# Kernel tuning notes

Hardware: AMD Instinct MI355X
Metric: run time of the kernel (lower is better)

## Reference

```python
import jax, jax.numpy as jnp
import numpy as np
from jax import lax

B, N, M = 16, 4096, 1024
RADII = [0.1, 0.2]
KS = [32, 64]
MLP_SPECS = [[64, 64, 128], [64, 96, 128]]
C_IN = 64 + 3  # use_xyz
EPS = 1e-5


def setup_inputs() -> dict:
    key = jax.random.key(0)
    ks = jax.random.split(key, 32)
    inp = {
        "pc": jax.random.uniform(ks[0], (B, 3, N), jnp.float32),
        "features": jax.random.normal(ks[1], (B, 64, N), jnp.float32),
    }
    ki = 2
    for i, spec in enumerate(MLP_SPECS):
        cin = C_IN
        for j, cout in enumerate(spec):
            inp[f"W{i}{j}"] = jax.random.normal(ks[ki], (cout, cin), jnp.float32) * (1.0 / np.sqrt(cin)); ki += 1
            inp[f"b{i}{j}"] = jnp.zeros((cout,), jnp.float32)
            inp[f"g{i}{j}"] = jnp.ones((cout,), jnp.float32)
            inp[f"be{i}{j}"] = jnp.zeros((cout,), jnp.float32)
            cin = cout
    return inp


def farthest_point_sampling(pc_t, m):
    # pc_t: [B, N, 3] -> [B, m] int32 indices. Sequential FPS via scan.
    b, n, _ = pc_t.shape
    init = (jnp.full((b, n), 1e10, pc_t.dtype), jnp.zeros((b,), jnp.int32))
    def step(carry, _):
        dmin, far = carry
        centroid = jnp.take_along_axis(pc_t, far[:, None, None], axis=1)  # [B,1,3]
        dist = jnp.sum((pc_t - centroid) ** 2, axis=-1)                    # [B,N]
        dmin = jnp.minimum(dmin, dist)
        nxt = jnp.argmax(dmin, axis=-1).astype(jnp.int32)
        return (dmin, nxt), far
    _, idxs = lax.scan(step, init, None, length=m)
    return idxs.T  # [B, m]


def ball_query(pc_t, centers_t, r, k):
    # pc_t: [B,N,3], centers_t: [B,M,3] -> [B,M,k] int32.
    # Original CUDA semantics: first k points (in index order) within radius;
    # pad with the first found index if fewer than k.
    n = pc_t.shape[1]
    d2 = jnp.sum((centers_t[:, :, None, :] - pc_t[:, None, :, :]) ** 2, axis=-1)  # [B,M,N]
    cand = jnp.where(d2 < r * r, jnp.arange(n, dtype=jnp.int32), jnp.int32(n))
    neg, _ = lax.top_k(-cand, k)   # k smallest candidate indices
    idx = -neg
    first = idx[:, :, :1]
    return jnp.where(idx == n, first, idx)


def group_points(feat, idx):
    # feat: [B,C,N], idx: [B,M,K] -> [B,C,M,K]
    return jax.vmap(lambda f, i: f[:, i])(feat, idx)


def _mlp_bn_relu(x, params):
    # x: [B,C,M,K]; 1x1 conv == channel matmul, BN over (B,M,K) (training stats), ReLU
    for (W, b, g, be) in params:
        x = jnp.einsum('oc,bcmk->bomk', W, x) + b[None, :, None, None]
        mu = jnp.mean(x, axis=(0, 2, 3), keepdims=True)
        var = jnp.var(x, axis=(0, 2, 3), keepdims=True)
        x = (x - mu) * lax.rsqrt(var + EPS) * g[None, :, None, None] + be[None, :, None, None]
        x = jax.nn.relu(x)
    return x


def _forward(pc, features, params):
    pc_t = pc.transpose(0, 2, 1)                       # [B,N,3]
    samp = farthest_point_sampling(pc_t, M)            # [B,M]
    new_pc = jnp.take_along_axis(pc, jnp.broadcast_to(samp[:, None, :], (B, 3, M)), axis=2)  # [B,3,M]
    new_pc_t = new_pc.transpose(0, 2, 1)               # [B,M,3]
    outs = []
    for i in range(len(RADII)):
        gidx = ball_query(pc_t, new_pc_t, RADII[i], KS[i])          # [B,M,K]
        xyz = group_points(pc, gidx) - new_pc[:, :, :, None]        # [B,3,M,K]
        grp = group_points(features, gidx)                          # [B,64,M,K]
        x = jnp.concatenate([xyz, grp], axis=1)                     # [B,67,M,K]
        x = _mlp_bn_relu(x, params[i])
        outs.append(jnp.max(x, axis=-1))                            # [B,Cout,M]
    return new_pc, jnp.concatenate(outs, axis=1)


def reference(pc, features,
              W00, b00, g00, be00, W01, b01, g01, be01, W02, b02, g02, be02,
              W10, b10, g10, be10, W11, b11, g11, be11, W12, b12, g12, be12):
    params = [
        [(W00, b00, g00, be00), (W01, b01, g01, be01), (W02, b02, g02, be02)],
        [(W10, b10, g10, be10), (W11, b11, g11, be11), (W12, b12, g12, be12)],
    ]
    return _forward(pc, features, params)
```

## Files before the change

### kernel.cpp

```cpp
#include <hip/hip_runtime.h>
#include <cstdio>
#include <cstdint>


constexpr int BATCH = 16, NPTS = 4096, MCTR = 1024;
constexpr int BM = BATCH * MCTR;
constexpr int NSLOT = 32;

typedef short bf16x8 __attribute__((ext_vector_type(8)));
typedef float f32x4  __attribute__((ext_vector_type(4)));
typedef float f32x2  __attribute__((ext_vector_type(2)));

__device__ __forceinline__ ushort f2bf(float f) {
  uint32_t u = __float_as_uint(f);
  u += 0x7fffu + ((u >> 16) & 1u);
  return (ushort)(u >> 16);
}
__device__ __forceinline__ uint32_t packbf(float a, float b) {
  return (uint32_t)f2bf(a) | ((uint32_t)f2bf(b) << 16);
}
__device__ __forceinline__ unsigned long long umax64(unsigned long long a,
                                                     unsigned long long b) {
  return (a > b) ? a : b;
}

template <int CTRL>
__device__ __forceinline__ unsigned long long dpp_max(unsigned long long k) {
  int lo = (int)(uint32_t)k, hi = (int)(uint32_t)(k >> 32);
  uint32_t plo = (uint32_t)__builtin_amdgcn_update_dpp(0, lo, CTRL, 0xf, 0xf, false);
  uint32_t phi = (uint32_t)__builtin_amdgcn_update_dpp(0, hi, CTRL, 0xf, 0xf, false);
  unsigned long long pk = ((unsigned long long)phi << 32) | plo;
  return (pk > k) ? pk : k;
}

__device__ __forceinline__ void fps_body(int b, int t, const float* __restrict__ pc,
                                         float* __restrict__ newpc_out,
                                         char* __restrict__ smem) {
  float* lX = (float*)smem;
  float* lY = lX + NPTS;
  float* lZ = lY + NPTS;
  int*   sampL = (int*)(smem + 3 * NPTS * 4);
  unsigned long long* wkey =
      (unsigned long long*)(smem + 3 * NPTS * 4 + MCTR * 4);
  const int lane = t & 63;
  const int w = t >> 6;
  const float* px = pc + (size_t)b * 3 * NPTS;
  f32x2 X2[8], Y2[8], Z2[8], D2[8];
#pragma unroll
  for (int j = 0; j < 16; j++) {
    int p = t + 256 * j;
    float x = px[p], y = px[NPTS + p], z = px[2 * NPTS + p];
    X2[j >> 1][j & 1] = x; Y2[j >> 1][j & 1] = y; Z2[j >> 1][j & 1] = z;
    D2[j >> 1][j & 1] = 1e10f;
    lX[p] = x; lY[p] = y; lZ[p] = z;
  }
  if (t == 0) sampL[0] = 0;
  __syncthreads();
  int far = 0;
  for (int it = 1; it < MCTR; it++) {
    float cx = lX[far], cy = lY[far], cz = lZ[far];
    float bv = -1.0f; int bi = 0;
    {
#pragma clang fp contract(off)
      f32x2 cx2 = {cx, cx}, cy2 = {cy, cy}, cz2 = {cz, cz};
#pragma unroll
      for (int j2 = 0; j2 < 8; j2++) {
        f32x2 dx = X2[j2] - cx2, dy = Y2[j2] - cy2, dz = Z2[j2] - cz2;
        f32x2 d = dx * dx + dy * dy + dz * dz;
        f32x2 dm;
        dm[0] = fminf(D2[j2][0], d[0]);
        dm[1] = fminf(D2[j2][1], d[1]);
        D2[j2] = dm;
        bool g0 = dm[0] > bv;
        bv = g0 ? dm[0] : bv; bi = g0 ? t + 256 * (2 * j2) : bi;
        bool g1 = dm[1] > bv;
        bv = g1 ? dm[1] : bv; bi = g1 ? t + 256 * (2 * j2 + 1) : bi;
      }
    }
    unsigned long long key =
        ((unsigned long long)__float_as_uint(bv) << 32) | (unsigned)(~bi);
    key = dpp_max<0xB1>(key);
    key = dpp_max<0x4E>(key);
    key = dpp_max<0x124>(key);
    key = dpp_max<0x128>(key);
    key = dpp_max<0x142>(key);
    key = dpp_max<0x143>(key);
    if (lane == 63) wkey[(it & 1) * 4 + w] = key;
    __syncthreads();
    const ulonglong2* kp = (const ulonglong2*)(wkey + (it & 1) * 4);
    ulonglong2 k0 = kp[0], k1 = kp[1];
    unsigned long long kk = umax64(umax64(k0.x, k0.y), umax64(k1.x, k1.y));
    far = (int)(~(unsigned)kk);
    if (t == 0) sampL[it] = far;
  }
  __syncthreads();
  float* npc = newpc_out + (size_t)b * 3 * MCTR;
  for (int m = t; m < MCTR; m += 256) {
    int f = sampL[m];
    npc[m] = lX[f]; npc[MCTR + m] = lY[f]; npc[2 * MCTR + m] = lZ[f];
  }
}

__device__ __forceinline__ void u_body(const float* __restrict__ feat,
                                       const float* __restrict__ W,
                                       const float* __restrict__ bias,
                                       ushort* __restrict__ Ub, int ub,
                                       char* __restrict__ smem) {
  float* wl = (float*)smem;
  int t = threadIdx.x;
#pragma unroll
  for (int i = 0; i < 16; i++) {
    int r = t + 256 * i;
    wl[r] = W[(r & 63) * 67 + 3 + (r >> 6)];
  }
  __syncthreads();
  int gid = ub * 256 + t;
  int b = gid >> 12, n = gid & 4095;
  float acc[64];
#pragma unroll
  for (int o = 0; o < 64; o++) acc[o] = bias[o];
  const float* fb = feat + (size_t)b * 64 * NPTS + n;
  for (int c = 0; c < 64; c++) {
    float x = fb[(size_t)c * NPTS];
    const f32x4* w4 = (const f32x4*)(wl + c * 64);
#pragma unroll
    for (int q = 0; q < 16; q++) {
      f32x4 wv = w4[q];
      acc[4 * q + 0] = fmaf(wv[0], x, acc[4 * q + 0]);
      acc[4 * q + 1] = fmaf(wv[1], x, acc[4 * q + 1]);
      acc[4 * q + 2] = fmaf(wv[2], x, acc[4 * q + 2]);
      acc[4 * q + 3] = fmaf(wv[3], x, acc[4 * q + 3]);
    }
  }
  uint4* o4 = (uint4*)(Ub + (size_t)gid * 64);
#pragma unroll
  for (int qq = 0; qq < 8; qq++)
    o4[qq] = make_uint4(packbf(acc[8*qq+0], acc[8*qq+1]), packbf(acc[8*qq+2], acc[8*qq+3]),
                        packbf(acc[8*qq+4], acc[8*qq+5]), packbf(acc[8*qq+6], acc[8*qq+7]));
}

__global__ __launch_bounds__(256) void fused_stageA(
    const float* __restrict__ pc, const float* __restrict__ feat,
    const float* __restrict__ W00, const float* __restrict__ b00,
    const float* __restrict__ W01, const float* __restrict__ W02,
    const float* __restrict__ W10, const float* __restrict__ b10,
    const float* __restrict__ W11, const float* __restrict__ W12,
    float* __restrict__ newpc_out, ushort* __restrict__ Ub0,
    ushort* __restrict__ Ub1, float* __restrict__ wt, ushort* __restrict__ wf) {
  __shared__ __align__(16) char smem[3 * NPTS * 4 + MCTR * 4 + 64];
  int bx = blockIdx.x, t = threadIdx.x;
  if (bx < 16) { fps_body(bx, t, pc, newpc_out, smem); return; }
  if (bx < 528) {
    int ub = bx - 16;
    if (ub < 256) u_body(feat, W00, b00, Ub0, ub, smem);
    else          u_body(feat, W10, b10, Ub1, ub - 256, smem);
    return;
  }
  int e = (bx - 528) * 256 + t;
  if (e < 4096) { wt[e] = W00[(e & 63) * 67 + 3 + (e >> 6)]; return; }
  if (e < 4288) { int r = e - 4096; wt[e] = W00[(r & 63) * 67 + (r >> 6)]; return; }
  if (e < 8384) { int r = e - 4288; wt[e] = W10[(r & 63) * 67 + 3 + (r >> 6)]; return; }
  if (e < 8576) { int r = e - 8384; wt[e] = W10[(r & 63) * 67 + (r >> 6)]; return; }
  int e2 = e - 8576;
  if (e2 >= 30720) return;
  const float* W; int CIN, MT, off;
  if (e2 < 4096)       { W = W01; CIN = 64; MT = 4; off = 0; }
  else if (e2 < 12288) { W = W02; CIN = 64; MT = 8; off = 4096; }
  else if (e2 < 18432) { W = W11; CIN = 64; MT = 6; off = 12288; }
  else                 { W = W12; CIN = 96; MT = 8; off = 18432; }
  int r = e2 - off;
  int j = r & 7, lane = (r >> 3) & 63, fm = r >> 9;
  int kc = fm / MT, mt = fm % MT;
  int out_ch = mt * 16 + (lane & 15);
  int in_ch  = kc * 32 + (lane >> 4) * 8 + j;
  wf[e2] = f2bf(W[out_ch * CIN + in_ch]);
}

template <int K>
__device__ __forceinline__ void ballq_body(int bx, const float* __restrict__ pc,
                                           const float* __restrict__ newpc,
                                           int* __restrict__ gidx, float r2) {
  int lane = threadIdx.x & 63;
  int wave = threadIdx.x >> 6;
  int center = bx * 4 + wave;
  int b = center >> 10, m = center & 1023;
  const float* nb = newpc + (size_t)b * 3 * MCTR + m;
  float cx = nb[0], cy = nb[MCTR], cz = nb[2 * MCTR];
  const float* px = pc + (size_t)b * 3 * NPTS;
  int cnt = 0;
  int firstn = 0x7fffffff;
  for (int chunk = 0; chunk < NPTS / 64 && cnt < K; chunk++) {
    int n = chunk * 64 + lane;
    float dx = __fsub_rn(cx, px[n]);
    float dy = __fsub_rn(cy, px[NPTS + n]);
    float dz = __fsub_rn(cz, px[2 * NPTS + n]);
    float d2 = __fadd_rn(__fadd_rn(__fmul_rn(dx, dx), __fmul_rn(dy, dy)), __fmul_rn(dz, dz));
    bool in = d2 < r2;
    unsigned long long ball = __ballot(in);
    int pos = cnt + (int)__popcll(ball & ((1ull << lane) - 1ull));
    if (in && pos < K) gidx[(size_t)center * K + pos] = n;
    if (in && pos == 0) firstn = n;
    cnt += (int)__popcll(ball);
  }
#pragma unroll
  for (int off = 32; off; off >>= 1) firstn = min(firstn, __shfl_xor(firstn, off));
  if (lane < K && lane >= cnt) gidx[(size_t)center * K + lane] = firstn;
}

__global__ __launch_bounds__(256) void ballq_fused(const float* __restrict__ pc,
                                                   const float* __restrict__ newpc,
                                                   int* __restrict__ gidx0,
                                                   int* __restrict__ gidx1,
                                                   float r2a, float r2b) {
  int bx = blockIdx.x;
  if (bx < BM / 4) ballq_body<32>(bx, pc, newpc, gidx0, r2a);
  else             ballq_body<64>(bx - BM / 4, pc, newpc, gidx1, r2b);
}

__device__ __forceinline__ void layer1_compute(const ushort* __restrict__ Ub,
                                               const float* __restrict__ pc,
                                               const float* __restrict__ newpc,
                                               const float* __restrict__ Wt1,
                                               int b, int m, int idx, float* v1) {
  float dx = pc[((size_t)b * 3 + 0) * NPTS + idx] - newpc[((size_t)b * 3 + 0) * MCTR + m];
  float dy = pc[((size_t)b * 3 + 1) * NPTS + idx] - newpc[((size_t)b * 3 + 1) * MCTR + m];
  float dz = pc[((size_t)b * 3 + 2) * NPTS + idx] - newpc[((size_t)b * 3 + 2) * MCTR + m];
  const uint4* u4 = (const uint4*)(Ub + (size_t)((b << 12) + idx) * 64);
#pragma unroll
  for (int qq = 0; qq < 8; qq++) {
    uint4 u = u4[qq];
    v1[8*qq+0] = __uint_as_float(u.x << 16);
    v1[8*qq+1] = __uint_as_float(u.x & 0xffff0000u);
    v1[8*qq+2] = __uint_as_float(u.y << 16);
    v1[8*qq+3] = __uint_as_float(u.y & 0xffff0000u);
    v1[8*qq+4] = __uint_as_float(u.z << 16);
    v1[8*qq+5] = __uint_as_float(u.z & 0xffff0000u);
    v1[8*qq+6] = __uint_as_float(u.w << 16);
    v1[8*qq+7] = __uint_as_float(u.w & 0xffff0000u);
  }
#pragma unroll
  for (int o = 0; o < 64; o++) v1[o] = fmaf(Wt1[o], dx, v1[o]);
#pragma unroll
  for (int o = 0; o < 64; o++) v1[o] = fmaf(Wt1[64 + o], dy, v1[o]);
#pragma unroll
  for (int o = 0; o < 64; o++) v1[o] = fmaf(Wt1[128 + o], dz, v1[o]);
}

__device__ __forceinline__ void wave_reduce32(const float* vals, float* tile, int t,
                                              float* swrow, int co) {
  float* myrow = tile + t * 32;
  int rsw = t & 31;
#pragma unroll
  for (int o = 0; o < 32; o++) myrow[o ^ rsw] = vals[o];
  __syncthreads();
  int lane = t & 63;
  int ch = lane & 31, sub = lane >> 5;
  const float* base = tile + (t & ~63) * 32;
  float s = 0.f, s2 = 0.f;
#pragma unroll
  for (int r = 0; r < 32; r++) {
    int row = sub * 32 + r;
    float v = base[row * 32 + (ch ^ (row & 31))];
    s += v; s2 = fmaf(v, v, s2);
  }
  float st = s + __shfl_xor(s, 32);
  float st2 = s2 + __shfl_xor(s2, 32);
  if (sub == 0) {
    swrow[co + ch] += st;
    swrow[128 + co + ch] += st2;
  }
  __syncthreads();
}

template <int K>
__device__ __forceinline__ void l1_body(
    int bx, const ushort* __restrict__ Ub, const float* __restrict__ pc,
    const float* __restrict__ newpc, const int* __restrict__ gidx,
    const float* __restrict__ Wt1, float* __restrict__ stats,
    float* tile, float* sAcc ) {
  const int t = threadIdx.x;
  const int w = t >> 6;
  const int p = bx * 128 + t;
  const int bm = p / K;
  const int b = bm >> 10, m = bm & 1023;
  const int idx = gidx[p];
  for (int i = t; i < 512; i += 128) sAcc[i] = 0.f;

  float v1[64];
  layer1_compute(Ub, pc, newpc, Wt1, b, m, idx, v1);

  wave_reduce32(v1,      tile, t, sAcc + w * 256, 0);
  wave_reduce32(v1 + 32, tile, t, sAcc + w * 256, 32);

  __syncthreads();
  float* dst = stats + (size_t)(bx & (NSLOT - 1)) * 128;
  for (int i = t; i < 64; i += 128) {
    atomicAdd(&dst[i],      sAcc[i]       + sAcc[256 + i]);
    atomicAdd(&dst[64 + i], sAcc[128 + i] + sAcc[256 + 128 + i]);
  }
}

__global__ __launch_bounds__(128, 2) void l1_fused(
    const ushort* __restrict__ Ub0, const ushort* __restrict__ Ub1,
    const float* __restrict__ pc, const float* __restrict__ newpc,
    const int* __restrict__ gidx0, const int* __restrict__ gidx1,
    const float* __restrict__ Wt1a, const float* __restrict__ Wt1b,
    float* __restrict__ st0, float* __restrict__ st1) {
  __shared__ float tile[128 * 32];
  __shared__ float sAccW[2][256];
  constexpr int NB0 = (BM * 32) / 128;
  int bx = blockIdx.x;
  if (bx < NB0) l1_body<32>(bx, Ub0, pc, newpc, gidx0, Wt1a, st0, tile, &sAccW[0][0]);
  else          l1_body<64>(bx - NB0, Ub1, pc, newpc, gidx1, Wt1b, st1, tile, &sAccW[0][0]);
}

template <int K, int C2, int NL>
__global__ __launch_bounds__(256, 2) void mfma_pass(
    const ushort* __restrict__ Ub, const float* __restrict__ pc,
    const float* __restrict__ newpc, const int* __restrict__ gidx,
    const float* __restrict__ Wt1,
    const ushort* __restrict__ W2f, const ushort* __restrict__ W3f,
    const float* __restrict__ b2, const float* __restrict__ b3,
    const float* __restrict__ cA1, const float* __restrict__ cC1,
    const float* __restrict__ cA2, const float* __restrict__ cC2,
    float* __restrict__ stats, float* __restrict__ maxbuf, float* __restrict__ minbuf) {
  constexpr int MT2 = C2 / 16, KC3 = C2 / 32;
  constexpr int CLs = (NL == 2) ? C2 : 128;
  constexpr int SSTR = CLs + 4;
  __shared__ __align__(16) ushort x1f[4][2][4][64][8];
  __shared__ __align__(16) ushort x2f[(NL == 3) ? 4 : 1][KC3][4][16][8];
  __shared__ __align__(16) ushort x3s[4][16][SSTR];
  __shared__ float sAccW[4][256];

  const int t = threadIdx.x, w = t >> 6, lane = t & 63;
  const int q = lane >> 4, n = lane & 15;
  const int p = blockIdx.x * 256 + t;
  const int bm = p / K;
  const int b = bm >> 10, m = bm & 1023;
  const int idx = gidx[p];

  {
    float v1[64];
    layer1_compute(Ub, pc, newpc, Wt1, b, m, idx, v1);
    int nw = t & 63;
#pragma unroll
    for (int g = 0; g < 8; g++) {
      uint32_t d0, d1, d2, d3;
      int c = g * 8;
      d0 = packbf(fmaxf(0.f, fmaf(cA1[c+0], v1[c+0], cC1[c+0])),
                  fmaxf(0.f, fmaf(cA1[c+1], v1[c+1], cC1[c+1])));
      d1 = packbf(fmaxf(0.f, fmaf(cA1[c+2], v1[c+2], cC1[c+2])),
                  fmaxf(0.f, fmaf(cA1[c+3], v1[c+3], cC1[c+3])));
      d2 = packbf(fmaxf(0.f, fmaf(cA1[c+4], v1[c+4], cC1[c+4])),
                  fmaxf(0.f, fmaf(cA1[c+5], v1[c+5], cC1[c+5])));
      d3 = packbf(fmaxf(0.f, fmaf(cA1[c+6], v1[c+6], cC1[c+6])),
                  fmaxf(0.f, fmaf(cA1[c+7], v1[c+7], cC1[c+7])));
      *(uint4*)&x1f[w][g >> 2][g & 3][nw][0] = make_uint4(d0, d1, d2, d3);
    }
  }
  asm volatile("s_waitcnt lgkmcnt(0)" ::: "memory");

  bf16x8 A2[2 * MT2];
#pragma unroll
  for (int i = 0; i < 2 * MT2; i++) A2[i] = *(const bf16x8*)(W2f + (i * 64 + lane) * 8);
  bf16x8 A3[(NL == 3) ? KC3 * 8 : 1];
  if (NL == 3) {
#pragma unroll
    for (int i = 0; i < KC3 * 8; i++) A3[i] = *(const bf16x8*)(W3f + (i * 64 + lane) * 8);
  }

  float sS0 = 0.f, sS1 = 0.f, sS20 = 0.f, sS21 = 0.f;
  float mx0 = -3.4e38f, mx1 = -3.4e38f, mn0 = 3.4e38f, mn1 = 3.4e38f;

#pragma unroll
  for (int tl = 0; tl < 4; tl++) {
    bf16x8 bf2[2];
#pragma unroll
    for (int kc = 0; kc < 2; kc++)
      bf2[kc] = *(const bf16x8*)&x1f[w][kc][q][tl * 16 + n][0];
    f32x4 acc2[MT2];
#pragma unroll
    for (int mt = 0; mt < MT2; mt++) acc2[mt] = *(const f32x4*)(b2 + mt * 16 + q * 4);
#pragma unroll
    for (int kc = 0; kc < 2; kc++)
#pragma unroll
      for (int mt = 0; mt < MT2; mt++)
        acc2[mt] = __builtin_amdgcn_mfma_f32_16x16x32_bf16(A2[kc * MT2 + mt], bf2[kc],
                                                           acc2[mt], 0, 0, 0);
    if (NL == 2) {
#pragma unroll
      for (int mt = 0; mt < MT2; mt++) {
        int ch0 = mt * 16 + q * 4;
        *(uint2*)&x3s[w][n][ch0] = make_uint2(packbf(acc2[mt][0], acc2[mt][1]),
                                              packbf(acc2[mt][2], acc2[mt][3]));
      }
    } else {
#pragma unroll
      for (int mt = 0; mt < MT2; mt++) {
        int ch0 = mt * 16 + q * 4;
        f32x4 ca = *(const f32x4*)(cA2 + ch0);
        f32x4 cc = *(const f32x4*)(cC2 + ch0);
        float r0 = fmaxf(0.f, fmaf(ca[0], acc2[mt][0], cc[0]));
        float r1 = fmaxf(0.f, fmaf(ca[1], acc2[mt][1], cc[1]));
        float r2 = fmaxf(0.f, fmaf(ca[2], acc2[mt][2], cc[2]));
        float r3 = fmaxf(0.f, fmaf(ca[3], acc2[mt][3], cc[3]));
        int kc2 = ch0 >> 5, q2 = (ch0 >> 3) & 3, j0 = ch0 & 7;
        *(uint2*)&x2f[w][kc2][q2][n][j0] = make_uint2(packbf(r0, r1), packbf(r2, r3));
      }
      asm volatile("s_waitcnt lgkmcnt(0)" ::: "memory");
      f32x4 acc3[8];
#pragma unroll
      for (int mt = 0; mt < 8; mt++) acc3[mt] = *(const f32x4*)(b3 + mt * 16 + q * 4);
#pragma unroll
      for (int kc = 0; kc < KC3; kc++) {
        bf16x8 bf3 = *(const bf16x8*)&x2f[w][kc][q][n][0];
#pragma unroll
        for (int mt = 0; mt < 8; mt++)
          acc3[mt] = __builtin_amdgcn_mfma_f32_16x16x32_bf16(A3[kc * 8 + mt], bf3,
                                                             acc3[mt], 0, 0, 0);
      }
#pragma unroll
      for (int mt = 0; mt < 8; mt++) {
        int ch0 = mt * 16 + q * 4;
        *(uint2*)&x3s[w][n][ch0] = make_uint2(packbf(acc3[mt][0], acc3[mt][1]),
                                              packbf(acc3[mt][2], acc3[mt][3]));
      }
    }
    asm volatile("s_waitcnt lgkmcnt(0)" ::: "memory");
    if (2 * lane < CLs) {
#pragma unroll
      for (int pos = 0; pos < 16; pos++) {
        uint32_t u = *(const uint32_t*)&x3s[w][pos][2 * lane];
        float v0 = __uint_as_float(u << 16);
        float v1v = __uint_as_float(u & 0xffff0000u);
        sS0 += v0;  sS20 = fmaf(v0, v0, sS20);
        sS1 += v1v; sS21 = fmaf(v1v, v1v, sS21);
        if (NL == 3) {
          mx0 = fmaxf(mx0, v0);  mn0 = fminf(mn0, v0);
          mx1 = fmaxf(mx1, v1v); mn1 = fminf(mn1, v1v);
        }
      }
    }
    if (NL == 3) {
      bool fl = (K == 64) ? (tl == 3) : ((tl & 1) == 1);
      if (fl) {
        int center = (K == 64) ? (blockIdx.x * 4 + w)
                               : (blockIdx.x * 8 + w * 2 + (tl >> 1));
        *(float2*)&maxbuf[(size_t)center * 128 + 2 * lane] = make_float2(mx0, mx1);
        *(float2*)&minbuf[(size_t)center * 128 + 2 * lane] = make_float2(mn0, mn1);
        mx0 = mx1 = -3.4e38f; mn0 = mn1 = 3.4e38f;
      }
    }
    asm volatile("s_waitcnt lgkmcnt(0)" ::: "memory");
  }

  {
    int ch = 2 * lane;
    if (ch < CLs) {
      sAccW[w][ch] = sS0;        sAccW[w][ch + 1] = sS1;
      sAccW[w][CLs + ch] = sS20; sAccW[w][CLs + ch + 1] = sS21;
    }
  }
  __syncthreads();
  float* dst = stats + (size_t)(blockIdx.x & (NSLOT - 1)) * (2 * CLs);
  for (int i = t; i < 2 * CLs; i += 256)
    atomicAdd(&dst[i], sAccW[0][i] + sAccW[1][i] + sAccW[2][i] + sAccW[3][i]);
}

__global__ void finalize2_kernel(const float* __restrict__ st0, const float* __restrict__ g0,
                                 const float* __restrict__ be0, float invP0,
                                 float* __restrict__ cAo0, float* __restrict__ cCo0, int C0,
                                 const float* __restrict__ st1, const float* __restrict__ g1,
                                 const float* __restrict__ be1, float invP1,
                                 float* __restrict__ cAo1, float* __restrict__ cCo1, int C1) {
  const float* st = blockIdx.x ? st1 : st0;
  const float* g  = blockIdx.x ? g1  : g0;
  const float* be = blockIdx.x ? be1 : be0;
  float invP = blockIdx.x ? invP1 : invP0;
  float* cA = blockIdx.x ? cAo1 : cAo0;
  float* cC = blockIdx.x ? cCo1 : cCo0;
  int C = blockIdx.x ? C1 : C0;
  int t = threadIdx.x;
  if (t < C) {
    float s = 0.f, s2 = 0.f;
    for (int sl = 0; sl < NSLOT; sl++) {
      s  += st[sl * 2 * C + t];
      s2 += st[sl * 2 * C + C + t];
    }
    float mu = s * invP;
    float var = fmaf(s2, invP, -(mu * mu));
    float a = g[t] / sqrtf(var + 1e-5f);
    cA[t] = a;
    cC[t] = fmaf(-a, mu, be[t]);
  }
}

__global__ __launch_bounds__(256) void outwrite_kernel(const float* __restrict__ maxbuf,
                                                       const float* __restrict__ minbuf,
                                                       const float* __restrict__ cA3,
                                                       const float* __restrict__ cC3,
                                                       float* __restrict__ out_feat, int chOff) {
  __shared__ float tile[64 * 130];
  int c0 = blockIdx.x * 64;
  int t = threadIdx.x;
#pragma unroll
  for (int i = 0; i < 32; i++) {
    int e = i * 256 + t;
    int lc = e >> 7, o = e & 127;
    float a = cA3[o];
    float v = (a >= 0.f) ? fmaf(a, maxbuf[(size_t)(c0 + lc) * 128 + o], cC3[o])
                         : fmaf(a, minbuf[(size_t)(c0 + lc) * 128 + o], cC3[o]);
    tile[lc * 130 + o] = fmaxf(v, 0.f);
  }
  __syncthreads();
  int b = c0 >> 10, m0 = c0 & 1023;
#pragma unroll
  for (int j = 0; j < 32; j++) {
    int e = j * 256 + t;
    int lm = e & 63, o = e >> 6;
    out_feat[((size_t)(b * 256 + chOff + o)) * MCTR + m0 + lm] = tile[lm * 130 + o];
  }
}

extern "C" void kernel_launch(void* const* d_in, const int* in_sizes, int n_in,
                              void* d_out, int out_size, void* d_ws, size_t ws_size,
                              hipStream_t stream) {
  (void)in_sizes; (void)n_in; (void)out_size;
  const float* pc   = (const float*)d_in[0];
  const float* feat = (const float*)d_in[1];
  const float *Wp[2][3], *bp[2][3], *gp[2][3], *bep[2][3];
  for (int s = 0; s < 2; s++)
    for (int l = 0; l < 3; l++) {
      int base = 2 + (s * 3 + l) * 4;
      Wp[s][l]  = (const float*)d_in[base + 0];
      bp[s][l]  = (const float*)d_in[base + 1];
      gp[s][l]  = (const float*)d_in[base + 2];
      bep[s][l] = (const float*)d_in[base + 3];
    }

  char* ws = (char*)d_ws;
  float*  statsR  = (float*) (ws + 0x10000);
  float*  coef    = (float*) (ws + 0x40000);
  float*  wt      = (float*) (ws + 0x42000);
  ushort* wf      = (ushort*)(ws + 0x50000);
  ushort* Ub0     = (ushort*)(ws + 0x100000);
  ushort* Ub1     = (ushort*)(ws + 0x900000);
  int*    gidx0   = (int*)   (ws + 0x1100000);
  int*    gidx1   = (int*)   (ws + 0x1300000);
  float*  maxbuf  = (float*) (ws + 0x1700000);
  float*  minbuf  = (float*) (ws + 0x1F00000);
  const unsigned long long WS_NEEDED = 0x2700000ULL;
  if (ws_size < WS_NEEDED) {
    fprintf(stderr, "[kernel] ws too small: %zu < %llu\n", ws_size, WS_NEEDED);
    return;
  }
  float* cf0 = coef, *cf1 = coef + 768;

  float* out_newpc = (float*)d_out;
  float* out_feat  = (float*)d_out + (size_t)BATCH * 3 * MCTR;

  const int P0 = BM * 32, P1 = BM * 64;
  const int LSTRIDE = NSLOT * 256;
  float* st10 = statsR + 0 * LSTRIDE, *st20 = statsR + 1 * LSTRIDE, *st30 = statsR + 2 * LSTRIDE;
  float* st11 = statsR + 3 * LSTRIDE, *st21 = statsR + 4 * LSTRIDE, *st31 = statsR + 5 * LSTRIDE;

  hipMemsetAsync(statsR, 0, 6 * NSLOT * 256 * sizeof(float), stream);
  fused_stageA<<<682, 256, 0, stream>>>(pc, feat,
                                        Wp[0][0], bp[0][0], Wp[0][1], Wp[0][2],
                                        Wp[1][0], bp[1][0], Wp[1][1], Wp[1][2],
                                        out_newpc, Ub0, Ub1, wt, wf);
  ballq_fused<<<BM / 2, 256, 0, stream>>>(pc, out_newpc, gidx0, gidx1,
                                          (float)(0.1 * 0.1), (float)(0.2 * 0.2));

  l1_fused<<<P0 / 128 + P1 / 128, 128, 0, stream>>>(Ub0, Ub1, pc, out_newpc,
                                                    gidx0, gidx1,
                                                    wt + 4096, wt + 8384, st10, st11);
  finalize2_kernel<<<2, 128, 0, stream>>>(st10, gp[0][0], bep[0][0], 1.0f / P0,
                                          cf0 + 0, cf0 + 128, 64,
                                          st11, gp[1][0], bep[1][0], 1.0f / P1,
                                          cf1 + 0, cf1 + 128, 64);

  mfma_pass<32, 64, 2><<<P0 / 256, 256, 0, stream>>>(Ub0, pc, out_newpc, gidx0,
      wt + 4096, wf + 0, wf + 4096, bp[0][1], bp[0][2],
      cf0 + 0, cf0 + 128, nullptr, nullptr, st20, nullptr, nullptr);
  mfma_pass<64, 96, 2><<<P1 / 256, 256, 0, stream>>>(Ub1, pc, out_newpc, gidx1,
      wt + 8384, wf + 12288, wf + 18432, bp[1][1], bp[1][2],
      cf1 + 0, cf1 + 128, nullptr, nullptr, st21, nullptr, nullptr);
  finalize2_kernel<<<2, 128, 0, stream>>>(st20, gp[0][1], bep[0][1], 1.0f / P0,
                                          cf0 + 256, cf0 + 384, 64,
                                          st21, gp[1][1], bep[1][1], 1.0f / P1,
                                          cf1 + 256, cf1 + 384, 96);

  mfma_pass<32, 64, 3><<<P0 / 256, 256, 0, stream>>>(Ub0, pc, out_newpc, gidx0,
      wt + 4096, wf + 0, wf + 4096, bp[0][1], bp[0][2],
      cf0 + 0, cf0 + 128, cf0 + 256, cf0 + 384, st30, maxbuf, minbuf);
  finalize2_kernel<<<1, 128, 0, stream>>>(st30, gp[0][2], bep[0][2], 1.0f / P0,
                                          cf0 + 512, cf0 + 640, 128,
                                          st30, gp[0][2], bep[0][2], 1.0f / P0,
                                          cf0 + 512, cf0 + 640, 128);
  outwrite_kernel<<<BM / 64, 256, 0, stream>>>(maxbuf, minbuf, cf0 + 512, cf0 + 640,
                                               out_feat, 0);

  mfma_pass<64, 96, 3><<<P1 / 256, 256, 0, stream>>>(Ub1, pc, out_newpc, gidx1,
      wt + 8384, wf + 12288, wf + 18432, bp[1][1], bp[1][2],
      cf1 + 0, cf1 + 128, cf1 + 256, cf1 + 384, st31, maxbuf, minbuf);
  finalize2_kernel<<<1, 128, 0, stream>>>(st31, gp[1][2], bep[1][2], 1.0f / P1,
                                          cf1 + 512, cf1 + 640, 128,
                                          st31, gp[1][2], bep[1][2], 1.0f / P1,
                                          cf1 + 512, cf1 + 640, 128);
  outwrite_kernel<<<BM / 64, 256, 0, stream>>>(maxbuf, minbuf, cf1 + 512, cf1 + 640,
                                               out_feat, 128);
}
```

Baseline: 1.239 ms.

## Overlap ball query with FPS via per-chunk flags and carry centroid coordinates

Ball-query blocks now run in the same launch as farthest point sampling. FPS publishes sampled centers in chunks of 128, and each chunk sets a release flag that ball-query waves spin on before reading. The FPS inner loop also carries the winning point's coordinates through a two-level reduction (16-lane DPP, then a cross-group DPP plus ballot and readlane), so the next centroid no longer needs an LDS lookup on the dependent path. The cost is extra select instructions per point, a larger LDS record, and spin-waiting blocks that could deadlock or take CU slots if the FPS blocks are not scheduled first.

After: 1.690 ms. +36.4%, slower.

```diff
diff --git a/kernel.cpp b/kernel.cpp
--- a/kernel.cpp
+++ b/kernel.cpp
@@ -18,10 +18,6 @@
 }
 __device__ __forceinline__ uint32_t packbf(float a, float b) {
   return (uint32_t)f2bf(a) | ((uint32_t)f2bf(b) << 16);
-}
-__device__ __forceinline__ unsigned long long umax64(unsigned long long a,
-                                                     unsigned long long b) {
-  return (a > b) ? a : b;
 }
 
 template <int CTRL>
@@ -35,13 +31,13 @@
 
 __device__ __forceinline__ void fps_body(int b, int t, const float* __restrict__ pc,
                                          float* __restrict__ newpc_out,
+                                         int* __restrict__ flags,
                                          char* __restrict__ smem) {
   float* lX = (float*)smem;
   float* lY = lX + NPTS;
   float* lZ = lY + NPTS;
   int*   sampL = (int*)(smem + 3 * NPTS * 4);
-  unsigned long long* wkey =
-      (unsigned long long*)(smem + 3 * NPTS * 4 + MCTR * 4);
+  char*  recs  = smem + 3 * NPTS * 4 + MCTR * 4;
   const int lane = t & 63;
   const int w = t >> 6;
   const float* px = pc + (size_t)b * 3 * NPTS;
@@ -56,10 +52,12 @@
   }
   if (t == 0) sampL[0] = 0;
   __syncthreads();
+  float cx = lX[0], cy = lY[0], cz = lZ[0];
   int far = 0;
+  float* npc = newpc_out + (size_t)b * 3 * MCTR;
   for (int it = 1; it < MCTR; it++) {
-    float cx = lX[far], cy = lY[far], cz = lZ[far];
     float bv = -1.0f; int bi = 0;
+    float bxc = 0.f, byc = 0.f, bzc = 0.f;
     {
 #pragma clang fp contract(off)
       f32x2 cx2 = {cx, cx}, cy2 = {cy, cy}, cz2 = {cz, cz};
@@ -73,31 +71,53 @@
         D2[j2] = dm;
         bool g0 = dm[0] > bv;
         bv = g0 ? dm[0] : bv; bi = g0 ? t + 256 * (2 * j2) : bi;
+        bxc = g0 ? X2[j2][0] : bxc; byc = g0 ? Y2[j2][0] : byc; bzc = g0 ? Z2[j2][0] : bzc;
         bool g1 = dm[1] > bv;
         bv = g1 ? dm[1] : bv; bi = g1 ? t + 256 * (2 * j2 + 1) : bi;
+        bxc = g1 ? X2[j2][1] : bxc; byc = g1 ? Y2[j2][1] : byc; bzc = g1 ? Z2[j2][1] : bzc;
       }
     }
     unsigned long long key =
         ((unsigned long long)__float_as_uint(bv) << 32) | (unsigned)(~bi);
-    key = dpp_max<0xB1>(key);
-    key = dpp_max<0x4E>(key);
-    key = dpp_max<0x124>(key);
-    key = dpp_max<0x128>(key);
-    key = dpp_max<0x142>(key);
-    key = dpp_max<0x143>(key);
-    if (lane == 63) wkey[(it & 1) * 4 + w] = key;
+    unsigned long long rk = key;
+    rk = dpp_max<0xB1>(rk);
+    rk = dpp_max<0x4E>(rk);
+    rk = dpp_max<0x124>(rk);
+    rk = dpp_max<0x128>(rk);
+    char* wb = recs + (it & 1) * 640 + (w * 4 + (lane >> 4)) * 40;
+    if (key == rk) {
+      *(unsigned long long*)wb = key;
+      *(float2*)(wb + 8) = make_float2(bxc, byc);
+      *(float*)(wb + 16) = bzc;
+    }
     __syncthreads();
-    const ulonglong2* kp = (const ulonglong2*)(wkey + (it & 1) * 4);
-    ulonglong2 k0 = kp[0], k1 = kp[1];
-    unsigned long long kk = umax64(umax64(k0.x, k0.y), umax64(k1.x, k1.y));
-    far = (int)(~(unsigned)kk);
+    const char* rb = recs + (it & 1) * 640 + (lane & 15) * 40;
+    unsigned long long myk = *(const unsigned long long*)rb;
+    float2 rxy = *(const float2*)(rb + 8);
+    float rz = *(const float*)(rb + 16);
+    unsigned long long km = myk;
+    km = dpp_max<0xB1>(km);
+    km = dpp_max<0x4E>(km);
+    km = dpp_max<0x124>(km);
+    km = dpp_max<0x128>(km);
+    unsigned long long wm = __ballot(myk == km);
+    int srcl = (int)__builtin_ctzll(wm);
+    cx = __uint_as_float((uint32_t)__builtin_amdgcn_readlane(__float_as_uint(rxy.x), srcl));
+    cy = __uint_as_float((uint32_t)__builtin_amdgcn_readlane(__float_as_uint(rxy.y), srcl));
+    cz = __uint_as_float((uint32_t)__builtin_amdgcn_readlane(__float_as_uint(rz), srcl));
+    far = (int)(~(unsigned)km);
     if (t == 0) sampL[it] = far;
-  }
-  __syncthreads();
-  float* npc = newpc_out + (size_t)b * 3 * MCTR;
-  for (int m = t; m < MCTR; m += 256) {
-    int f = sampL[m];
-    npc[m] = lX[f]; npc[MCTR + m] = lY[f]; npc[2 * MCTR + m] = lZ[f];
+    if ((it & 127) == 127) {
+      if (t < 128) {
+        int s = (it & ~127) + t;
+        int f = (t == 127) ? far : sampL[s];
+        npc[s] = lX[f]; npc[MCTR + s] = lY[f]; npc[2 * MCTR + s] = lZ[f];
+      }
+      __syncthreads();
+      if (t == 0)
+        __hip_atomic_store(&flags[b * 8 + (it >> 7)], 1, __ATOMIC_RELEASE,
+                           __HIP_MEMORY_SCOPE_AGENT);
+    }
   }
 }
 
@@ -139,51 +159,18 @@
                         packbf(acc[8*qq+4], acc[8*qq+5]), packbf(acc[8*qq+6], acc[8*qq+7]));
 }
 
-__global__ __launch_bounds__(256) void fused_stageA(
-    const float* __restrict__ pc, const float* __restrict__ feat,
-    const float* __restrict__ W00, const float* __restrict__ b00,
-    const float* __restrict__ W01, const float* __restrict__ W02,
-    const float* __restrict__ W10, const float* __restrict__ b10,
-    const float* __restrict__ W11, const float* __restrict__ W12,
-    float* __restrict__ newpc_out, ushort* __restrict__ Ub0,
-    ushort* __restrict__ Ub1, float* __restrict__ wt, ushort* __restrict__ wf) {
-  __shared__ __align__(16) char smem[3 * NPTS * 4 + MCTR * 4 + 64];
-  int bx = blockIdx.x, t = threadIdx.x;
-  if (bx < 16) { fps_body(bx, t, pc, newpc_out, smem); return; }
-  if (bx < 528) {
-    int ub = bx - 16;
-    if (ub < 256) u_body(feat, W00, b00, Ub0, ub, smem);
-    else          u_body(feat, W10, b10, Ub1, ub - 256, smem);
-    return;
-  }
-  int e = (bx - 528) * 256 + t;
-  if (e < 4096) { wt[e] = W00[(e & 63) * 67 + 3 + (e >> 6)]; return; }
-  if (e < 4288) { int r = e - 4096; wt[e] = W00[(r & 63) * 67 + (r >> 6)]; return; }
-  if (e < 8384) { int r = e - 4288; wt[e] = W10[(r & 63) * 67 + 3 + (r >> 6)]; return; }
-  if (e < 8576) { int r = e - 8384; wt[e] = W10[(r & 63) * 67 + (r >> 6)]; return; }
-  int e2 = e - 8576;
-  if (e2 >= 30720) return;
-  const float* W; int CIN, MT, off;
-  if (e2 < 4096)       { W = W01; CIN = 64; MT = 4; off = 0; }
-  else if (e2 < 12288) { W = W02; CIN = 64; MT = 8; off = 4096; }
-  else if (e2 < 18432) { W = W11; CIN = 64; MT = 6; off = 12288; }
-  else                 { W = W12; CIN = 96; MT = 8; off = 18432; }
-  int r = e2 - off;
-  int j = r & 7, lane = (r >> 3) & 63, fm = r >> 9;
-  int kc = fm / MT, mt = fm % MT;
-  int out_ch = mt * 16 + (lane & 15);
-  int in_ch  = kc * 32 + (lane >> 4) * 8 + j;
-  wf[e2] = f2bf(W[out_ch * CIN + in_ch]);
-}
-
 template <int K>
 __device__ __forceinline__ void ballq_body(int bx, const float* __restrict__ pc,
                                            const float* __restrict__ newpc,
-                                           int* __restrict__ gidx, float r2) {
+                                           int* __restrict__ gidx, float r2,
+                                           const int* __restrict__ flags) {
   int lane = threadIdx.x & 63;
   int wave = threadIdx.x >> 6;
   int center = bx * 4 + wave;
   int b = center >> 10, m = center & 1023;
+  while (__hip_atomic_load(&flags[b * 8 + (m >> 7)], __ATOMIC_ACQUIRE,
+                           __HIP_MEMORY_SCOPE_AGENT) == 0)
+    __builtin_amdgcn_s_sleep(8);
   const float* nb = newpc + (size_t)b * 3 * MCTR + m;
   float cx = nb[0], cy = nb[MCTR], cz = nb[2 * MCTR];
   const float* px = pc + (size_t)b * 3 * NPTS;
@@ -207,14 +194,49 @@
   if (lane < K && lane >= cnt) gidx[(size_t)center * K + lane] = firstn;
 }
 
-__global__ __launch_bounds__(256) void ballq_fused(const float* __restrict__ pc,
-                                                   const float* __restrict__ newpc,
-                                                   int* __restrict__ gidx0,
-                                                   int* __restrict__ gidx1,
-                                                   float r2a, float r2b) {
-  int bx = blockIdx.x;
-  if (bx < BM / 4) ballq_body<32>(bx, pc, newpc, gidx0, r2a);
-  else             ballq_body<64>(bx - BM / 4, pc, newpc, gidx1, r2b);
+__global__ __launch_bounds__(256) void fused_stageA(
+    const float* __restrict__ pc, const float* __restrict__ feat,
+    const float* __restrict__ W00, const float* __restrict__ b00,
+    const float* __restrict__ W01, const float* __restrict__ W02,
+    const float* __restrict__ W10, const float* __restrict__ b10,
+    const float* __restrict__ W11, const float* __restrict__ W12,
+    float* __restrict__ newpc_out, ushort* __restrict__ Ub0,
+    ushort* __restrict__ Ub1, float* __restrict__ wt, ushort* __restrict__ wf,
+    int* __restrict__ gidx0, int* __restrict__ gidx1,
+    int* __restrict__ flags, float r2a, float r2b) {
+  __shared__ __align__(16) char smem[3 * NPTS * 4 + MCTR * 4 + 1280];
+  int bx = blockIdx.x, t = threadIdx.x;
+  if (bx < 16) { fps_body(bx, t, pc, newpc_out, flags, smem); return; }
+  if (bx < 528) {
+    int ub = bx - 16;
+    if (ub < 256) u_body(feat, W00, b00, Ub0, ub, smem);
+    else          u_body(feat, W10, b10, Ub1, ub - 256, smem);
+    return;
+  }
+  if (bx < 682) {
+    int e = (bx - 528) * 256 + t;
+    if (e < 4096) { wt[e] = W00[(e & 63) * 67 + 3 + (e >> 6)]; return; }
+    if (e < 4288) { int r = e - 4096; wt[e] = W00[(r & 63) * 67 + (r >> 6)]; return; }
+    if (e < 8384) { int r = e - 4288; wt[e] = W10[(r & 63) * 67 + 3 + (r >> 6)]; return; }
+    if (e < 8576) { int r = e - 8384; wt[e] = W10[(r & 63) * 67 + (r >> 6)]; return; }
+    int e2 = e - 8576;
+    if (e2 >= 30720) return;
+    const float* W; int CIN, MT, off;
+    if (e2 < 4096)       { W = W01; CIN = 64; MT = 4; off = 0; }
+    else if (e2 < 12288) { W = W02; CIN = 64; MT = 8; off = 4096; }
+    else if (e2 < 18432) { W = W11; CIN = 64; MT = 6; off = 12288; }
+    else                 { W = W12; CIN = 96; MT = 8; off = 18432; }
+    int r = e2 - off;
+    int j = r & 7, lane = (r >> 3) & 63, fm = r >> 9;
+    int kc = fm / MT, mt = fm % MT;
+    int out_ch = mt * 16 + (lane & 15);
+    int in_ch  = kc * 32 + (lane >> 4) * 8 + j;
+    wf[e2] = f2bf(W[out_ch * CIN + in_ch]);
+    return;
+  }
+  int bq = bx - 682;
+  if (bq < BM / 4) ballq_body<32>(bq, pc, newpc_out, gidx0, r2a, flags);
+  else             ballq_body<64>(bq - BM / 4, pc, newpc_out, gidx1, r2b, flags);
 }
 
 __device__ __forceinline__ void layer1_compute(const ushort* __restrict__ Ub,
@@ -539,6 +561,7 @@
     }
 
   char* ws = (char*)d_ws;
+  int*    flags   = (int*)   (ws + 0x8000);
   float*  statsR  = (float*) (ws + 0x10000);
   float*  coef    = (float*) (ws + 0x40000);
   float*  wt      = (float*) (ws + 0x42000);
@@ -564,13 +587,14 @@
   float* st10 = statsR + 0 * LSTRIDE, *st20 = statsR + 1 * LSTRIDE, *st30 = statsR + 2 * LSTRIDE;
   float* st11 = statsR + 3 * LSTRIDE, *st21 = statsR + 4 * LSTRIDE, *st31 = statsR + 5 * LSTRIDE;
 
+  hipMemsetAsync(flags, 0, 16 * 8 * sizeof(int), stream);
   hipMemsetAsync(statsR, 0, 6 * NSLOT * 256 * sizeof(float), stream);
-  fused_stageA<<<682, 256, 0, stream>>>(pc, feat,
+  fused_stageA<<<682 + BM / 2, 256, 0, stream>>>(pc, feat,
                                         Wp[0][0], bp[0][0], Wp[0][1], Wp[0][2],
                                         Wp[1][0], bp[1][0], Wp[1][1], Wp[1][2],
-                                        out_newpc, Ub0, Ub1, wt, wf);
-  ballq_fused<<<BM / 2, 256, 0, stream>>>(pc, out_newpc, gidx0, gidx1,
-                                          (float)(0.1 * 0.1), (float)(0.2 * 0.2));
+                                        out_newpc, Ub0, Ub1, wt, wf,
+                                        gidx0, gidx1, flags,
+                                        (float)(0.1 * 0.1), (float)(0.2 * 0.2));
 
   l1_fused<<<P0 / 128 + P1 / 128, 128, 0, stream>>>(Ub0, Ub1, pc, out_newpc,
                                                     gidx0, gidx1,
```

## Merge per-branch MLP passes into single launches and store max/min in bf16

Applied to the files above, without the earlier changes.

The two radius branches' layer-2 and layer-3 MFMA passes are merged into single kernels that dispatch on block index, using a shared-memory buffer sized for the larger branch. The finalize and output-write steps are likewise merged, so fewer launches run and small branches no longer leave the GPU idle in their tails. The per-center max/min buffers are now stored as bf16 instead of fp32, with separate buffers per branch, which halves that traffic. The risk is lost precision in the output max values and higher shared-memory use for the smaller branch, which can lower occupancy.

Measured after the change: 1.488 ms. +20.1%, slower.

```diff
diff --git a/kernel.cpp b/kernel.cpp
--- a/kernel.cpp
+++ b/kernel.cpp
@@ -315,26 +315,34 @@
 }
 
 template <int K, int C2, int NL>
-__global__ __launch_bounds__(256, 2) void mfma_pass(
-    const ushort* __restrict__ Ub, const float* __restrict__ pc,
+__device__ __forceinline__ void mfma_body(
+    int bx, const ushort* __restrict__ Ub, const float* __restrict__ pc,
     const float* __restrict__ newpc, const int* __restrict__ gidx,
     const float* __restrict__ Wt1,
     const ushort* __restrict__ W2f, const ushort* __restrict__ W3f,
     const float* __restrict__ b2, const float* __restrict__ b3,
     const float* __restrict__ cA1, const float* __restrict__ cC1,
     const float* __restrict__ cA2, const float* __restrict__ cC2,
-    float* __restrict__ stats, float* __restrict__ maxbuf, float* __restrict__ minbuf) {
+    float* __restrict__ stats, ushort* __restrict__ maxbuf,
+    ushort* __restrict__ minbuf, char* __restrict__ smem) {
   constexpr int MT2 = C2 / 16, KC3 = C2 / 32;
   constexpr int CLs = (NL == 2) ? C2 : 128;
   constexpr int SSTR = CLs + 4;
-  __shared__ __align__(16) ushort x1f[4][2][4][64][8];
-  __shared__ __align__(16) ushort x2f[(NL == 3) ? 4 : 1][KC3][4][16][8];
-  __shared__ __align__(16) ushort x3s[4][16][SSTR];
-  __shared__ float sAccW[4][256];
+  using X1F = ushort[4][2][4][64][8];
+  using X2F = ushort[(NL == 3) ? 4 : 1][KC3][4][16][8];
+  using X3S = ushort[4][16][SSTR];
+  using SACC = float[4][256];
+  constexpr size_t OFF_X2F = sizeof(X1F);
+  constexpr size_t OFF_X3S = OFF_X2F + sizeof(X2F);
+  constexpr size_t OFF_SACC = OFF_X3S + sizeof(X3S);
+  X1F& x1f = *(X1F*)smem;
+  X2F& x2f = *(X2F*)(smem + OFF_X2F);
+  X3S& x3s = *(X3S*)(smem + OFF_X3S);
+  SACC& sAccW = *(SACC*)(smem + OFF_SACC);
 
   const int t = threadIdx.x, w = t >> 6, lane = t & 63;
   const int q = lane >> 4, n = lane & 15;
-  const int p = blockIdx.x * 256 + t;
+  const int p = bx * 256 + t;
   const int bm = p / K;
   const int b = bm >> 10, m = bm & 1023;
   const int idx = gidx[p];
@@ -444,10 +452,10 @@
     if (NL == 3) {
       bool fl = (K == 64) ? (tl == 3) : ((tl & 1) == 1);
       if (fl) {
-        int center = (K == 64) ? (blockIdx.x * 4 + w)
-                               : (blockIdx.x * 8 + w * 2 + (tl >> 1));
-        *(float2*)&maxbuf[(size_t)center * 128 + 2 * lane] = make_float2(mx0, mx1);
-        *(float2*)&minbuf[(size_t)center * 128 + 2 * lane] = make_float2(mn0, mn1);
+        int center = (K == 64) ? (bx * 4 + w)
+                               : (bx * 8 + w * 2 + (tl >> 1));
+        *(uint32_t*)&maxbuf[(size_t)center * 128 + 2 * lane] = packbf(mx0, mx1);
+        *(uint32_t*)&minbuf[(size_t)center * 128 + 2 * lane] = packbf(mn0, mn1);
         mx0 = mx1 = -3.4e38f; mn0 = mn1 = 3.4e38f;
       }
     }
@@ -462,9 +470,55 @@
     }
   }
   __syncthreads();
-  float* dst = stats + (size_t)(blockIdx.x & (NSLOT - 1)) * (2 * CLs);
+  float* dst = stats + (size_t)(bx & (NSLOT - 1)) * (2 * CLs);
   for (int i = t; i < 2 * CLs; i += 256)
     atomicAdd(&dst[i], sAccW[0][i] + sAccW[1][i] + sAccW[2][i] + sAccW[3][i]);
+}
+
+constexpr int NB2_0 = (BM * 32) / 256;
+constexpr int NB2_1 = (BM * 64) / 256;
+
+__global__ __launch_bounds__(256, 2) void mfma2_fused(
+    const ushort* __restrict__ Ub0, const ushort* __restrict__ Ub1,
+    const float* __restrict__ pc, const float* __restrict__ newpc,
+    const int* __restrict__ gidx0, const int* __restrict__ gidx1,
+    const float* __restrict__ wt, const ushort* __restrict__ wf,
+    const float* __restrict__ b01, const float* __restrict__ b11,
+    const float* __restrict__ coef, float* __restrict__ st20,
+    float* __restrict__ st21) {
+  __shared__ __align__(16) char smem[52736];
+  int bx = blockIdx.x;
+  if (bx < NB2_0)
+    mfma_body<32, 64, 2>(bx, Ub0, pc, newpc, gidx0, wt + 4096, wf + 0, wf + 4096,
+                         b01, nullptr, coef + 0, coef + 128, nullptr, nullptr,
+                         st20, nullptr, nullptr, smem);
+  else
+    mfma_body<64, 96, 2>(bx - NB2_0, Ub1, pc, newpc, gidx1, wt + 8384, wf + 12288,
+                         wf + 18432, b11, nullptr, coef + 768, coef + 768 + 128,
+                         nullptr, nullptr, st21, nullptr, nullptr, smem);
+}
+
+__global__ __launch_bounds__(256, 2) void mfma3_fused(
+    const ushort* __restrict__ Ub0, const ushort* __restrict__ Ub1,
+    const float* __restrict__ pc, const float* __restrict__ newpc,
+    const int* __restrict__ gidx0, const int* __restrict__ gidx1,
+    const float* __restrict__ wt, const ushort* __restrict__ wf,
+    const float* __restrict__ b01, const float* __restrict__ b02,
+    const float* __restrict__ b11, const float* __restrict__ b12,
+    const float* __restrict__ coef, float* __restrict__ st30,
+    float* __restrict__ st31,
+    ushort* __restrict__ mx0, ushort* __restrict__ mn0,
+    ushort* __restrict__ mx1, ushort* __restrict__ mn1) {
+  __shared__ __align__(16) char smem[78336];
+  int bx = blockIdx.x;
+  if (bx < NB2_0)
+    mfma_body<32, 64, 3>(bx, Ub0, pc, newpc, gidx0, wt + 4096, wf + 0, wf + 4096,
+                         b01, b02, coef + 0, coef + 128, coef + 256, coef + 384,
+                         st30, mx0, mn0, smem);
+  else
+    mfma_body<64, 96, 3>(bx - NB2_0, Ub1, pc, newpc, gidx1, wt + 8384, wf + 12288,
+                         wf + 18432, b11, b12, coef + 768, coef + 768 + 128,
+                         coef + 768 + 256, coef + 768 + 384, st31, mx1, mn1, smem);
 }
 
 __global__ void finalize2_kernel(const float* __restrict__ st0, const float* __restrict__ g0,
@@ -495,21 +549,30 @@
   }
 }
 
-__global__ __launch_bounds__(256) void outwrite_kernel(const float* __restrict__ maxbuf,
-                                                       const float* __restrict__ minbuf,
-                                                       const float* __restrict__ cA3,
-                                                       const float* __restrict__ cC3,
-                                                       float* __restrict__ out_feat, int chOff) {
+__global__ __launch_bounds__(256) void outwrite_fused(
+    const ushort* __restrict__ mx0buf, const ushort* __restrict__ mn0buf,
+    const ushort* __restrict__ mx1buf, const ushort* __restrict__ mn1buf,
+    const float* __restrict__ coef, float* __restrict__ out_feat) {
   __shared__ float tile[64 * 130];
-  int c0 = blockIdx.x * 64;
+  int bx = blockIdx.x;
+  const ushort* mxb; const ushort* mnb; const float* cA3; const float* cC3;
+  int chOff, c0;
+  if (bx < BM / 64) {
+    mxb = mx0buf; mnb = mn0buf; cA3 = coef + 512; cC3 = coef + 640;
+    chOff = 0; c0 = bx * 64;
+  } else {
+    mxb = mx1buf; mnb = mn1buf; cA3 = coef + 768 + 512; cC3 = coef + 768 + 640;
+    chOff = 128; c0 = (bx - BM / 64) * 64;
+  }
   int t = threadIdx.x;
 #pragma unroll
   for (int i = 0; i < 32; i++) {
     int e = i * 256 + t;
     int lc = e >> 7, o = e & 127;
     float a = cA3[o];
-    float v = (a >= 0.f) ? fmaf(a, maxbuf[(size_t)(c0 + lc) * 128 + o], cC3[o])
-                         : fmaf(a, minbuf[(size_t)(c0 + lc) * 128 + o], cC3[o]);
+    float mv = __uint_as_float(((uint32_t)mxb[(size_t)(c0 + lc) * 128 + o]) << 16);
+    float nv = __uint_as_float(((uint32_t)mnb[(size_t)(c0 + lc) * 128 + o]) << 16);
+    float v = (a >= 0.f) ? fmaf(a, mv, cC3[o]) : fmaf(a, nv, cC3[o]);
     tile[lc * 130 + o] = fmaxf(v, 0.f);
   }
   __syncthreads();
@@ -547,8 +610,10 @@
   ushort* Ub1     = (ushort*)(ws + 0x900000);
   int*    gidx0   = (int*)   (ws + 0x1100000);
   int*    gidx1   = (int*)   (ws + 0x1300000);
-  float*  maxbuf  = (float*) (ws + 0x1700000);
-  float*  minbuf  = (float*) (ws + 0x1F00000);
+  ushort* mxb0    = (ushort*)(ws + 0x1700000);
+  ushort* mnb0    = (ushort*)(ws + 0x1B00000);
+  ushort* mxb1    = (ushort*)(ws + 0x1F00000);
+  ushort* mnb1    = (ushort*)(ws + 0x2300000);
   const unsigned long long WS_NEEDED = 0x2700000ULL;
   if (ws_size < WS_NEEDED) {
     fprintf(stderr, "[kernel] ws too small: %zu < %llu\n", ws_size, WS_NEEDED);
@@ -580,34 +645,23 @@
                                           st11, gp[1][0], bep[1][0], 1.0f / P1,
                                           cf1 + 0, cf1 + 128, 64);
 
-  mfma_pass<32, 64, 2><<<P0 / 256, 256, 0, stream>>>(Ub0, pc, out_newpc, gidx0,
-      wt + 4096, wf + 0, wf + 4096, bp[0][1], bp[0][2],
-      cf0 + 0, cf0 + 128, nullptr, nullptr, st20, nullptr, nullptr);
-  mfma_pass<64, 96, 2><<<P1 / 256, 256, 0, stream>>>(Ub1, pc, out_newpc, gidx1,
-      wt + 8384, wf + 12288, wf + 18432, bp[1][1], bp[1][2],
-      cf1 + 0, cf1 + 128, nullptr, nullptr, st21, nullptr, nullptr);
+  mfma2_fused<<<NB2_0 + NB2_1, 256, 0, stream>>>(Ub0, Ub1, pc, out_newpc,
+                                                 gidx0, gidx1, wt, wf,
+                                                 bp[0][1], bp[1][1], coef, st20, st21);
   finalize2_kernel<<<2, 128, 0, stream>>>(st20, gp[0][1], bep[0][1], 1.0f / P0,
                                           cf0 + 256, cf0 + 384, 64,
                                           st21, gp[1][1], bep[1][1], 1.0f / P1,
                                           cf1 + 256, cf1 + 384, 96);
 
-  mfma_pass<32, 64, 3><<<P0 / 256, 256, 0, stream>>>(Ub0, pc, out_newpc, gidx0,
-      wt + 4096, wf + 0, wf + 4096, bp[0][1], bp[0][2],
-      cf0 + 0, cf0 + 128, cf0 + 256, cf0 + 384, st30, maxbuf, minbuf);
-  finalize2_kernel<<<1, 128, 0, stream>>>(st30, gp[0][2], bep[0][2], 1.0f / P0,
+  mfma3_fused<<<NB2_0 + NB2_1, 256, 0, stream>>>(Ub0, Ub1, pc, out_newpc,
+                                                 gidx0, gidx1, wt, wf,
+                                                 bp[0][1], bp[0][2], bp[1][1], bp[1][2],
+                                                 coef, st30, st31,
+                                                 mxb0, mnb0, mxb1, mnb1);
+  finalize2_kernel<<<2, 128, 0, stream>>>(st30, gp[0][2], bep[0][2], 1.0f / P0,
                                           cf0 + 512, cf0 + 640, 128,
-                                          st30, gp[0][2], bep[0][2], 1.0f / P0,
-                                          cf0 + 512, cf0 + 640, 128);
-  outwrite_kernel<<<BM / 64, 256, 0, stream>>>(maxbuf, minbuf, cf0 + 512, cf0 + 640,
-                                               out_feat, 0);
-
-  mfma_pass<64, 96, 3><<<P1 / 256, 256, 0, stream>>>(Ub1, pc, out_newpc, gidx1,
-      wt + 8384, wf + 12288, wf + 18432, bp[1][1], bp[1][2],
-      cf1 + 0, cf1 + 128, cf1 + 256, cf1 + 384, st31, maxbuf, minbuf);
-  finalize2_kernel<<<1, 128, 0, stream>>>(st31, gp[1][2], bep[1][2], 1.0f / P1,
-                                          cf1 + 512, cf1 + 640, 128,
                                           st31, gp[1][2], bep[1][2], 1.0f / P1,
                                           cf1 + 512, cf1 + 640, 128);
-  outwrite_kernel<<<BM / 64, 256, 0, stream>>>(maxbuf, minbuf, cf1 + 512, cf1 + 640,
-                                               out_feat, 128);
-}
+  outwrite_fused<<<2 * (BM / 64), 256, 0, stream>>>(mxb0, mnb0, mxb1, mnb1,
+                                                    coef, out_feat);
+}
```
